# Optimization experiments

Hardware: AMD Instinct MI355X
Metric: run time of the kernel (lower is better)

## Reference

```python
import jax, jax.numpy as jnp
import numpy as np

B, N, D, H = 16, 256, 512, 8
DK = D // H          # 64
DIM_G = 64           # trigonometric geometry embedding dim
WAVE_LEN = 1000.0


def box_relational_embedding(boxes):
    # boxes: [B, N, 4] = (x_min, y_min, x_max, y_max)
    x_min, y_min, x_max, y_max = jnp.split(boxes, 4, axis=-1)  # each [B,N,1]
    cx = ((x_min + x_max) * 0.5)[..., 0]   # [B,N]
    cy = ((y_min + y_max) * 0.5)[..., 0]
    w = (x_max - x_min + 1.0)[..., 0]
    h = (y_max - y_min + 1.0)[..., 0]
    # pairwise deltas, normalized by the *row* box size (as in the torch code)
    dx = jnp.log(jnp.clip(jnp.abs((cx[:, :, None] - cx[:, None, :]) / w[:, :, None]), 1e-3))
    dy = jnp.log(jnp.clip(jnp.abs((cy[:, :, None] - cy[:, None, :]) / h[:, :, None]), 1e-3))
    dw = jnp.log(w[:, :, None] / w[:, None, :])
    dh = jnp.log(h[:, :, None] / h[:, None, :])
    pos = jnp.stack([dx, dy, dw, dh], axis=-1)  # [B,N,N,4]
    # trig embedding: freq per (dim_g/8) channels
    feat_range = jnp.arange(DIM_G // 8, dtype=pos.dtype) / (DIM_G / 8.0)
    dim_mat = 1.0 / jnp.power(WAVE_LEN, feat_range)               # [8]
    mul = (100.0 * pos)[..., None] * dim_mat                      # [B,N,N,4,8]
    mul = mul.reshape(mul.shape[:3] + (-1,))                      # [B,N,N,32]
    return jnp.concatenate([jnp.sin(mul), jnp.cos(mul)], axis=-1)  # [B,N,N,64]


def setup_inputs() -> dict:
    key = jax.random.key(0)
    ks = jax.random.split(key, 16)
    inp = {
        'input_query': jax.random.normal(ks[0], (B, N, D), jnp.float32),
        'input_key': jax.random.normal(ks[1], (B, N, D), jnp.float32),
        'input_value': jax.random.normal(ks[2], (B, N, D), jnp.float32),
    }
    # valid boxes: x_max > x_min, y_max > y_min
    xm = jax.random.uniform(ks[3], (B, N, 1)) * 800.0
    ym = jax.random.uniform(ks[4], (B, N, 1)) * 800.0
    bw = jax.random.uniform(ks[5], (B, N, 1)) * 120.0 + 5.0
    bh = jax.random.uniform(ks[6], (B, N, 1)) * 120.0 + 5.0
    inp['input_box'] = jnp.concatenate([xm, ym, xm + bw, ym + bh], axis=-1)
    s = 1.0 / np.sqrt(D)
    inp['Wq'] = jax.random.normal(ks[7], (D, D), jnp.float32) * s
    inp['bq'] = jnp.zeros((D,), jnp.float32)
    inp['Wk'] = jax.random.normal(ks[8], (D, D), jnp.float32) * s
    inp['bk'] = jnp.zeros((D,), jnp.float32)
    inp['Wv'] = jax.random.normal(ks[9], (D, D), jnp.float32) * s
    inp['bv'] = jnp.zeros((D,), jnp.float32)
    inp['Wo'] = jax.random.normal(ks[10], (D, D), jnp.float32) * s
    inp['bo'] = jnp.zeros((D,), jnp.float32)
    inp['Wg'] = jax.random.normal(ks[11], (H, DIM_G), jnp.float32) * (1.0 / np.sqrt(DIM_G))
    inp['bg'] = jnp.zeros((H,), jnp.float32)
    return inp


def reference(input_query, input_key, input_value, input_box,
              Wq, bq, Wk, bk, Wv, bv, Wo, bo, Wg, bg):
    nb = input_query.shape[0]
    geo = box_relational_embedding(input_box)                     # [B,N,N,64]
    wg = jax.nn.relu(jnp.einsum('bijg,hg->bhij', geo, Wg) + bg[None, :, None, None])
    def proj(x, W, b):
        return (x @ W + b).reshape(nb, -1, H, DK).transpose(0, 2, 1, 3)  # [B,H,N,dk]
    q = proj(input_query, Wq, bq)
    k = proj(input_key, Wk, bk)
    v = proj(input_value, Wv, bv)
    scores = jnp.einsum('bhid,bhjd->bhij', q, k) / np.sqrt(DK)    # [B,H,N,N]
    w_mn = jax.nn.softmax(jnp.log(jnp.clip(wg, 1e-6)) + scores, axis=-1)
    out = jnp.einsum('bhij,bhjd->bhid', w_mn, v)                  # [B,H,N,dk]
    out = out.transpose(0, 2, 1, 3).reshape(nb, -1, H * DK)       # [B,N,D]
    return out @ Wo + bo
```

## Files before the change

kernel.cpp:

```cpp
#include <hip/hip_runtime.h>
#include <hip/hip_bf16.h>

#define B_ 16
#define N_ 256
#define D_ 512
#define H_ 8
#define DK_ 64

typedef unsigned short u16;
typedef __attribute__((ext_vector_type(8))) short bf16x8;
typedef __attribute__((ext_vector_type(4))) float f32x4;

__device__ __forceinline__ float bf2f(u16 u) {
    union { unsigned int i; float f; } v;
    v.i = ((unsigned int)u) << 16;
    return v.f;
}
__device__ __forceinline__ u16 f2bf(float f) {
    union { float f; unsigned int i; } v;
    v.f = f;
    unsigned int x = v.i;
    unsigned int r = (x >> 16) & 1u;
    x += 0x7fffu + r;
    return (u16)(x >> 16);
}

__global__ __launch_bounds__(256) void k_prep(const float* __restrict__ box,
                                              const float* __restrict__ Wg,
                                              const float* __restrict__ bg,
                                              u16* __restrict__ Sg,
                                              const float* __restrict__ W0,
                                              const float* __restrict__ W1,
                                              const float* __restrict__ W2,
                                              const float* __restrict__ W3,
                                              u16* __restrict__ Wt) {
    const int tid = threadIdx.x;
    if (blockIdx.x < 4096) {
        __shared__ float sWg[8][64];
        __shared__ float sbg[8];
        if (tid < 8) sbg[tid] = bg[tid];
        { int e = tid; sWg[e >> 6][e & 63] = Wg[e];
          e = tid + 256; sWg[e >> 6][e & 63] = Wg[e]; }
        const int bi = blockIdx.x, b = bi >> 8;
        float4 bxi = *(const float4*)&box[(size_t)bi * 4];
        float4 bxj = *(const float4*)&box[(size_t)(b * N_ + tid) * 4];
        __syncthreads();
        float cxi = (bxi.x + bxi.z) * 0.5f, cyi = (bxi.y + bxi.w) * 0.5f;
        float wi = bxi.z - bxi.x + 1.0f, hi = bxi.w - bxi.y + 1.0f;
        float cxj = (bxj.x + bxj.z) * 0.5f, cyj = (bxj.y + bxj.w) * 0.5f;
        float wj = bxj.z - bxj.x + 1.0f, hj = bxj.w - bxj.y + 1.0f;
        float pos[4];
        pos[0] = __logf(fmaxf(fabsf((cxi - cxj) / wi), 1e-3f));
        pos[1] = __logf(fmaxf(fabsf((cyi - cyj) / hi), 1e-3f));
        pos[2] = __logf(wi / wj);
        pos[3] = __logf(hi / hj);
        const float dm[8] = {1.0f, 0.42169650342858224f, 0.1778279410038923f,
                             0.07498942093324559f, 0.03162277660168379f,
                             0.013335214321633241f, 0.005623413251903491f,
                             0.0023713737056616554f};
        const float inv2pi = 0.15915494309189535f;
        float acc[8];
#pragma unroll
        for (int h = 0; h < 8; ++h) acc[h] = sbg[h];
#pragma unroll
        for (int t = 0; t < 4; ++t) {
            float base = 100.0f * pos[t];
#pragma unroll
            for (int f = 0; f < 8; ++f) {
                float rev = base * dm[f] * inv2pi;
                rev = rev - floorf(rev);
                float sn = __builtin_amdgcn_sinf(rev);
                float cs = __builtin_amdgcn_cosf(rev);
                int idx = t * 8 + f;
#pragma unroll
                for (int h = 0; h < 8; ++h)
                    acc[h] += sWg[h][idx] * sn + sWg[h][idx + 32] * cs;
            }
        }
        const int i = bi & 255;
#pragma unroll
        for (int h = 0; h < 8; ++h)
            Sg[(((size_t)(b * H_ + h) * N_) + i) * N_ + tid] =
                f2bf(__logf(fmaxf(acc[h], 1e-6f)));
    } else {
        __shared__ float tt[32][33];
        int t = blockIdx.x - 4096;
        int z = t >> 8, yb = (t >> 4) & 15, xb = t & 15;
        const float* W = (z == 0) ? W0 : (z == 1) ? W1 : (z == 2) ? W2 : W3;
        u16* dst = Wt + (size_t)z * 262144;
        const int kb = yb * 32, nb = xb * 32;
#pragma unroll
        for (int r = 0; r < 4; ++r) {
            int p = r * 256 + tid;
            tt[p >> 5][p & 31] = W[(size_t)(kb + (p >> 5)) * 512 + nb + (p & 31)];
        }
        __syncthreads();
#pragma unroll
        for (int r = 0; r < 4; ++r) {
            int p = r * 256 + tid;
            dst[(size_t)(nb + (p >> 5)) * 512 + kb + (p & 31)] = f2bf(tt[p & 31][p >> 5]);
        }
    }
}

__global__ __launch_bounds__(256) void k_gemm_qkv(const float* __restrict__ Xq,
                                                  const float* __restrict__ Xk,
                                                  const float* __restrict__ Xv,
                                                  const u16* __restrict__ Wtb,
                                                  const float* __restrict__ bq,
                                                  const float* __restrict__ bk,
                                                  const float* __restrict__ bv,
                                                  u16* __restrict__ qkv) {
    const int z = blockIdx.z;
    const float* A = (z == 0) ? Xq : (z == 1) ? Xk : Xv;
    const u16* Wt = Wtb + (size_t)z * 262144;
    const float* bias = (z == 0) ? bq : (z == 1) ? bk : bv;
    u16* dst = qkv + (size_t)z * 2097152;

    __shared__ u16 As[2][64][72];
    __shared__ u16 Bs[2][64][72];
    const int tid = threadIdx.x;
    const int n0 = blockIdx.x * 64, m0 = blockIdx.y * 64;
    const int wid = tid >> 6, lane = tid & 63;
    const int wm = (wid & 1) * 32, wn = (wid >> 1) * 32;
    const int lr = lane & 15, lk8 = (lane >> 4) * 8, quad4 = (lane >> 4) * 4;

    f32x4 acc[2][2];
#pragma unroll
    for (int mi = 0; mi < 2; ++mi)
#pragma unroll
        for (int ni = 0; ni < 2; ++ni) acc[mi][ni] = (f32x4){0.f, 0.f, 0.f, 0.f};

    float4 raf[4];
    ushort4 rb[4];
#pragma unroll
    for (int r = 0; r < 4; ++r) {
        int p = r * 256 + tid, row = p >> 4, c4 = (p & 15) * 4;
        raf[r] = *(const float4*)&A[(size_t)(m0 + row) * 512 + c4];
        rb[r] = *(const ushort4*)&Wt[(size_t)(n0 + row) * 512 + c4];
    }
#pragma unroll
    for (int r = 0; r < 4; ++r) {
        int p = r * 256 + tid, row = p >> 4, c4 = (p & 15) * 4;
        ushort4 ab;
        ab.x = f2bf(raf[r].x); ab.y = f2bf(raf[r].y);
        ab.z = f2bf(raf[r].z); ab.w = f2bf(raf[r].w);
        *(ushort4*)&As[0][row][c4] = ab;
        *(ushort4*)&Bs[0][row][c4] = rb[r];
    }
    __syncthreads();
    for (int it = 0; it < 8; ++it) {
        const int cur = it & 1;
        if (it < 7) {
            int k0n = (it + 1) * 64;
#pragma unroll
            for (int r = 0; r < 4; ++r) {
                int p = r * 256 + tid, row = p >> 4, c4 = (p & 15) * 4;
                raf[r] = *(const float4*)&A[(size_t)(m0 + row) * 512 + k0n + c4];
                rb[r] = *(const ushort4*)&Wt[(size_t)(n0 + row) * 512 + k0n + c4];
            }
        }
#pragma unroll
        for (int ks = 0; ks < 64; ks += 32) {
            bf16x8 af[2], bfx[2];
#pragma unroll
            for (int mi = 0; mi < 2; ++mi)
                af[mi] = *(const bf16x8*)&As[cur][wm + mi * 16 + lr][ks + lk8];
#pragma unroll
            for (int ni = 0; ni < 2; ++ni)
                bfx[ni] = *(const bf16x8*)&Bs[cur][wn + ni * 16 + lr][ks + lk8];
#pragma unroll
            for (int mi = 0; mi < 2; ++mi)
#pragma unroll
                for (int ni = 0; ni < 2; ++ni)
                    acc[mi][ni] = __builtin_amdgcn_mfma_f32_16x16x32_bf16(
                        af[mi], bfx[ni], acc[mi][ni], 0, 0, 0);
        }
        if (it < 7) {
#pragma unroll
            for (int r = 0; r < 4; ++r) {
                int p = r * 256 + tid, row = p >> 4, c4 = (p & 15) * 4;
                ushort4 ab;
                ab.x = f2bf(raf[r].x); ab.y = f2bf(raf[r].y);
                ab.z = f2bf(raf[r].z); ab.w = f2bf(raf[r].w);
                *(ushort4*)&As[1 - cur][row][c4] = ab;
                *(ushort4*)&Bs[1 - cur][row][c4] = rb[r];
            }
            __syncthreads();
        }
    }
    u16* bounce = &As[0][0][0];
    const float scale = (z == 0) ? 0.125f : 1.0f;
    const int h = n0 >> 6, b = m0 >> 8, rrb = m0 & 255;
    if (z == 2) {
#pragma unroll
        for (int mi = 0; mi < 2; ++mi)
#pragma unroll
            for (int ni = 0; ni < 2; ++ni) {
                int cn = wn + ni * 16 + lr;
                float bb = bias[n0 + cn];
#pragma unroll
                for (int reg = 0; reg < 4; ++reg) {
                    int rm = wm + mi * 16 + quad4 + reg;
                    bounce[cn * 72 + rm] = f2bf(acc[mi][ni][reg] + bb);
                }
            }
        __syncthreads();
#pragma unroll
        for (int r = 0; r < 4; ++r) {
            int p = r * 256 + tid, dn = p >> 4, c4 = (p & 15) * 4;
            *(ushort4*)&dst[(((size_t)(b * H_ + h) * DK_) + dn) * N_ + rrb + c4] =
                *(const ushort4*)&bounce[dn * 72 + c4];
        }
    } else {
#pragma unroll
        for (int mi = 0; mi < 2; ++mi)
#pragma unroll
            for (int ni = 0; ni < 2; ++ni) {
                int cn = wn + ni * 16 + lr;
                float bb = bias[n0 + cn];
#pragma unroll
                for (int reg = 0; reg < 4; ++reg) {
                    int rm = wm + mi * 16 + quad4 + reg;
                    bounce[rm * 72 + cn] = f2bf((acc[mi][ni][reg] + bb) * scale);
                }
            }
        __syncthreads();
#pragma unroll
        for (int r = 0; r < 4; ++r) {
            int p = r * 256 + tid, rm = p >> 4, c4 = (p & 15) * 4;
            *(ushort4*)&dst[(((size_t)(b * H_ + h) * N_) + rrb + rm) * DK_ + c4] =
                *(const ushort4*)&bounce[rm * 72 + c4];
        }
    }
}

__global__ __launch_bounds__(256) void k_gemm_out(const u16* __restrict__ Ab,
                                                  const u16* __restrict__ Wt,
                                                  const float* __restrict__ bias,
                                                  float* __restrict__ outp) {
    __shared__ u16 As[2][64][72];
    __shared__ u16 Bs[2][64][72];
    const int tid = threadIdx.x;
    const int n0 = blockIdx.x * 64, m0 = blockIdx.y * 64;
    const int wid = tid >> 6, lane = tid & 63;
    const int wm = (wid & 1) * 32, wn = (wid >> 1) * 32;
    const int lr = lane & 15, lk8 = (lane >> 4) * 8;
    f32x4 acc[2][2];
#pragma unroll
    for (int mi = 0; mi < 2; ++mi)
#pragma unroll
        for (int ni = 0; ni < 2; ++ni) acc[mi][ni] = (f32x4){0.f, 0.f, 0.f, 0.f};
    ushort4 ra[4], rb[4];
#pragma unroll
    for (int r = 0; r < 4; ++r) {
        int p = r * 256 + tid, row = p >> 4, c4 = (p & 15) * 4;
        ra[r] = *(const ushort4*)&Ab[(size_t)(m0 + row) * 512 + c4];
        rb[r] = *(const ushort4*)&Wt[(size_t)(n0 + row) * 512 + c4];
    }
#pragma unroll
    for (int r = 0; r < 4; ++r) {
        int p = r * 256 + tid, row = p >> 4, c4 = (p & 15) * 4;
        *(ushort4*)&As[0][row][c4] = ra[r];
        *(ushort4*)&Bs[0][row][c4] = rb[r];
    }
    __syncthreads();
    for (int it = 0; it < 8; ++it) {
        const int cur = it & 1;
        if (it < 7) {
            int k0n = (it + 1) * 64;
#pragma unroll
            for (int r = 0; r < 4; ++r) {
                int p = r * 256 + tid, row = p >> 4, c4 = (p & 15) * 4;
                ra[r] = *(const ushort4*)&Ab[(size_t)(m0 + row) * 512 + k0n + c4];
                rb[r] = *(const ushort4*)&Wt[(size_t)(n0 + row) * 512 + k0n + c4];
            }
        }
#pragma unroll
        for (int ks = 0; ks < 64; ks += 32) {
            bf16x8 af[2], bfx[2];
#pragma unroll
            for (int mi = 0; mi < 2; ++mi)
                af[mi] = *(const bf16x8*)&As[cur][wm + mi * 16 + lr][ks + lk8];
#pragma unroll
            for (int ni = 0; ni < 2; ++ni)
                bfx[ni] = *(const bf16x8*)&Bs[cur][wn + ni * 16 + lr][ks + lk8];
#pragma unroll
            for (int mi = 0; mi < 2; ++mi)
#pragma unroll
                for (int ni = 0; ni < 2; ++ni)
                    acc[mi][ni] = __builtin_amdgcn_mfma_f32_16x16x32_bf16(
                        af[mi], bfx[ni], acc[mi][ni], 0, 0, 0);
        }
        if (it < 7) {
#pragma unroll
            for (int r = 0; r < 4; ++r) {
                int p = r * 256 + tid, row = p >> 4, c4 = (p & 15) * 4;
                *(ushort4*)&As[1 - cur][row][c4] = ra[r];
                *(ushort4*)&Bs[1 - cur][row][c4] = rb[r];
            }
            __syncthreads();
        }
    }
#pragma unroll
    for (int mi = 0; mi < 2; ++mi)
#pragma unroll
        for (int ni = 0; ni < 2; ++ni) {
            int col = n0 + wn + ni * 16 + lr;
            float bb = bias[col];
#pragma unroll
            for (int reg = 0; reg < 4; ++reg) {
                int m = m0 + wm + mi * 16 + (lane >> 4) * 4 + reg;
                outp[(size_t)m * 512 + col] = acc[mi][ni][reg] + bb;
            }
        }
}

__global__ __launch_bounds__(256) void k_attn(const u16* __restrict__ qh,
                                              const u16* __restrict__ kh,
                                              const u16* __restrict__ vhT,
                                              const u16* __restrict__ Sg,
                                              u16* __restrict__ attnb) {
    __shared__ __align__(16) unsigned char smem[40960];
    u16* sQ = (u16*)smem;
    u16* sP = (u16*)(smem + 4608);
    u16* sK = (u16*)(smem + 21504);
    u16* sVt = (u16*)(smem + 21504);
    float* sRedM = (float*)(smem + 39936);
    float* sRedS = (float*)(smem + 40448);

    const int tid = threadIdx.x;
    const int i0 = blockIdx.x * 32;
    const int bh = blockIdx.y;
    const int b = bh >> 3, h = bh & 7;
    const int wid = tid >> 6, lane = tid & 63;
    const int lr = lane & 15, lk8 = (lane >> 4) * 8, quad4 = (lane >> 4) * 4;

#pragma unroll
    for (int r = 0; r < 2; ++r) {
        int p = r * 256 + tid, i = p >> 4, d0 = (p & 15) * 4;
        *(ushort4*)&sQ[i * 72 + d0] =
            *(const ushort4*)&qh[((size_t)bh * N_ + i0 + i) * DK_ + d0];
    }
#pragma unroll
    for (int r = 0; r < 8; ++r) {
        int p = r * 256 + tid, row = p >> 6, jc = (p & 63) * 4;
        *(ushort4*)&sP[row * 264 + jc] =
            *(const ushort4*)&Sg[(((size_t)bh * N_) + i0 + row) * N_ + jc];
    }
#pragma unroll
    for (int r = 0; r < 8; ++r) {
        int p = r * 256 + tid, j = p >> 4, d0 = (p & 15) * 4;
        *(ushort4*)&sK[j * 72 + d0] =
            *(const ushort4*)&kh[((size_t)bh * N_ + j) * DK_ + d0];
    }
    __syncthreads();

    ushort4 kpre[8];
#pragma unroll
    for (int r = 0; r < 8; ++r) {
        int p = r * 256 + tid, j = p >> 4, d0 = (p & 15) * 4;
        kpre[r] = *(const ushort4*)&kh[((size_t)bh * N_ + 128 + j) * DK_ + d0];
    }
    f32x4 acc[2][2][2];
#pragma unroll
    for (int c = 0; c < 2; ++c)
#pragma unroll
        for (int mi = 0; mi < 2; ++mi)
#pragma unroll
            for (int ni = 0; ni < 2; ++ni) acc[c][mi][ni] = (f32x4){0.f, 0.f, 0.f, 0.f};
#pragma unroll
    for (int ks = 0; ks < 64; ks += 32) {
        bf16x8 af[2], bfx[2];
#pragma unroll
        for (int mi = 0; mi < 2; ++mi)
            af[mi] = *(const bf16x8*)&sQ[(mi * 16 + lr) * 72 + ks + lk8];
#pragma unroll
        for (int ni = 0; ni < 2; ++ni)
            bfx[ni] = *(const bf16x8*)&sK[(wid * 32 + ni * 16 + lr) * 72 + ks + lk8];
#pragma unroll
        for (int mi = 0; mi < 2; ++mi)
#pragma unroll
            for (int ni = 0; ni < 2; ++ni)
                acc[0][mi][ni] = __builtin_amdgcn_mfma_f32_16x16x32_bf16(
                    af[mi], bfx[ni], acc[0][mi][ni], 0, 0, 0);
    }
    __syncthreads();
#pragma unroll
    for (int r = 0; r < 8; ++r) {
        int p = r * 256 + tid, j = p >> 4, d0 = (p & 15) * 4;
        *(ushort4*)&sK[j * 72 + d0] = kpre[r];
    }
    __syncthreads();
#pragma unroll
    for (int ks = 0; ks < 64; ks += 32) {
        bf16x8 af[2], bfx[2];
#pragma unroll
        for (int mi = 0; mi < 2; ++mi)
            af[mi] = *(const bf16x8*)&sQ[(mi * 16 + lr) * 72 + ks + lk8];
#pragma unroll
        for (int ni = 0; ni < 2; ++ni)
            bfx[ni] = *(const bf16x8*)&sK[(wid * 32 + ni * 16 + lr) * 72 + ks + lk8];
#pragma unroll
        for (int mi = 0; mi < 2; ++mi)
#pragma unroll
            for (int ni = 0; ni < 2; ++ni)
                acc[1][mi][ni] = __builtin_amdgcn_mfma_f32_16x16x32_bf16(
                    af[mi], bfx[ni], acc[1][mi][ni], 0, 0, 0);
    }
    __syncthreads();

#pragma unroll
    for (int r = 0; r < 8; ++r) {
        int p = r * 256 + tid, d = p >> 5, jc = (p & 31) * 4;
        *(ushort4*)&sVt[d * 136 + jc] =
            *(const ushort4*)&vhT[(((size_t)bh * DK_) + d) * N_ + jc];
    }
#pragma unroll
    for (int c = 0; c < 2; ++c)
#pragma unroll
        for (int mi = 0; mi < 2; ++mi)
#pragma unroll
            for (int ni = 0; ni < 2; ++ni) {
                int col = c * 128 + wid * 32 + ni * 16 + lr;
#pragma unroll
                for (int reg = 0; reg < 4; ++reg) {
                    int row = mi * 16 + quad4 + reg;
                    acc[c][mi][ni][reg] += bf2f(sP[row * 264 + col]);
                }
            }
    float mrow[2][4];
#pragma unroll
    for (int mi = 0; mi < 2; ++mi)
#pragma unroll
        for (int reg = 0; reg < 4; ++reg) {
            float m = acc[0][mi][0][reg];
            m = fmaxf(m, acc[0][mi][1][reg]);
            m = fmaxf(m, acc[1][mi][0][reg]);
            m = fmaxf(m, acc[1][mi][1][reg]);
#pragma unroll
            for (int off = 1; off <= 8; off <<= 1) m = fmaxf(m, __shfl_xor(m, off, 64));
            mrow[mi][reg] = m;
        }
    if (lr == 0) {
#pragma unroll
        for (int mi = 0; mi < 2; ++mi)
#pragma unroll
            for (int reg = 0; reg < 4; ++reg)
                sRedM[(mi * 16 + quad4 + reg) * 4 + wid] = mrow[mi][reg];
    }
    __syncthreads();
    float gm[2][4], sl[2][4];
#pragma unroll
    for (int mi = 0; mi < 2; ++mi)
#pragma unroll
        for (int reg = 0; reg < 4; ++reg) {
            float4 mm = *(const float4*)&sRedM[(mi * 16 + quad4 + reg) * 4];
            gm[mi][reg] = fmaxf(fmaxf(mm.x, mm.y), fmaxf(mm.z, mm.w));
            sl[mi][reg] = 0.f;
        }
#pragma unroll
    for (int c = 0; c < 2; ++c)
#pragma unroll
        for (int mi = 0; mi < 2; ++mi)
#pragma unroll
            for (int ni = 0; ni < 2; ++ni)
#pragma unroll
                for (int reg = 0; reg < 4; ++reg) {
                    float e = __expf(acc[c][mi][ni][reg] - gm[mi][reg]);
                    acc[c][mi][ni][reg] = e;
                    sl[mi][reg] += e;
                }
#pragma unroll
    for (int mi = 0; mi < 2; ++mi)
#pragma unroll
        for (int reg = 0; reg < 4; ++reg) {
            float s = sl[mi][reg];
#pragma unroll
            for (int off = 1; off <= 8; off <<= 1) s += __shfl_xor(s, off, 64);
            sl[mi][reg] = s;
        }
    if (lr == 0) {
#pragma unroll
        for (int mi = 0; mi < 2; ++mi)
#pragma unroll
            for (int reg = 0; reg < 4; ++reg)
                sRedS[(mi * 16 + quad4 + reg) * 4 + wid] = sl[mi][reg];
    }
    __syncthreads();
#pragma unroll
    for (int mi = 0; mi < 2; ++mi)
#pragma unroll
        for (int reg = 0; reg < 4; ++reg) {
            float4 ss = *(const float4*)&sRedS[(mi * 16 + quad4 + reg) * 4];
            gm[mi][reg] = 1.0f / (ss.x + ss.y + ss.z + ss.w);
        }
#pragma unroll
    for (int c = 0; c < 2; ++c)
#pragma unroll
        for (int mi = 0; mi < 2; ++mi)
#pragma unroll
            for (int ni = 0; ni < 2; ++ni) {
                int col = c * 128 + wid * 32 + ni * 16 + lr;
#pragma unroll
                for (int reg = 0; reg < 4; ++reg) {
                    int row = mi * 16 + quad4 + reg;
                    sP[row * 264 + col] = f2bf(acc[c][mi][ni][reg] * gm[mi][reg]);
                }
            }
    __syncthreads();

    f32x4 o[2];
    o[0] = (f32x4){0.f, 0.f, 0.f, 0.f};
    o[1] = (f32x4){0.f, 0.f, 0.f, 0.f};
#pragma unroll
    for (int k0 = 0; k0 < 128; k0 += 32) {
        bf16x8 bfx = *(const bf16x8*)&sVt[(wid * 16 + lr) * 136 + k0 + lk8];
#pragma unroll
        for (int mi = 0; mi < 2; ++mi) {
            bf16x8 af = *(const bf16x8*)&sP[(mi * 16 + lr) * 264 + k0 + lk8];
            o[mi] = __builtin_amdgcn_mfma_f32_16x16x32_bf16(af, bfx, o[mi], 0, 0, 0);
        }
    }
    __syncthreads();
#pragma unroll
    for (int r = 0; r < 8; ++r) {
        int p = r * 256 + tid, d = p >> 5, jc = (p & 31) * 4;
        *(ushort4*)&sVt[d * 136 + jc] =
            *(const ushort4*)&vhT[(((size_t)bh * DK_) + d) * N_ + 128 + jc];
    }
    __syncthreads();
#pragma unroll
    for (int k0 = 0; k0 < 128; k0 += 32) {
        bf16x8 bfx = *(const bf16x8*)&sVt[(wid * 16 + lr) * 136 + k0 + lk8];
#pragma unroll
        for (int mi = 0; mi < 2; ++mi) {
            bf16x8 af = *(const bf16x8*)&sP[(mi * 16 + lr) * 264 + 128 + k0 + lk8];
            o[mi] = __builtin_amdgcn_mfma_f32_16x16x32_bf16(af, bfx, o[mi], 0, 0, 0);
        }
    }
#pragma unroll
    for (int mi = 0; mi < 2; ++mi)
#pragma unroll
        for (int reg = 0; reg < 4; ++reg) {
            int row = mi * 16 + quad4 + reg;
            attnb[((size_t)(b * N_ + i0 + row)) * D_ + h * 64 + wid * 16 + lr] =
                f2bf(o[mi][reg]);
        }
}

extern "C" void kernel_launch(void* const* d_in, const int* in_sizes, int n_in,
                              void* d_out, int out_size, void* d_ws, size_t ws_size,
                              hipStream_t stream) {
    const float* Xq = (const float*)d_in[0];
    const float* Xk = (const float*)d_in[1];
    const float* Xv = (const float*)d_in[2];
    const float* box = (const float*)d_in[3];
    const float* Wq = (const float*)d_in[4];
    const float* bq = (const float*)d_in[5];
    const float* Wk = (const float*)d_in[6];
    const float* bk = (const float*)d_in[7];
    const float* Wv = (const float*)d_in[8];
    const float* bv = (const float*)d_in[9];
    const float* Wo = (const float*)d_in[10];
    const float* bo = (const float*)d_in[11];
    const float* Wg = (const float*)d_in[12];
    const float* bg = (const float*)d_in[13];
    float* out = (float*)d_out;

    u16* ws16 = (u16*)d_ws;
    u16* qkv = ws16;
    u16* qh = qkv;
    u16* kh = qkv + 2097152;
    u16* vhT = qkv + 4194304;
    u16* Sg = ws16 + 6291456;
    u16* attnb = ws16 + 14680064;
    u16* Wt = ws16 + 16777216;

    dim3 blk(256);
    k_prep<<<dim3(5120), blk, 0, stream>>>(box, Wg, bg, Sg, Wq, Wk, Wv, Wo, Wt);
    k_gemm_qkv<<<dim3(8, 64, 3), blk, 0, stream>>>(Xq, Xk, Xv, Wt, bq, bk, bv, qkv);
    k_attn<<<dim3(8, 128), blk, 0, stream>>>(qh, kh, vhT, Sg, attnb);
    k_gemm_out<<<dim3(8, 64), blk, 0, stream>>>(attnb, Wt + 3 * 262144, bo, out);
}
```

Baseline: 179.5 us.

## Enlarge GEMM M-tile to 128 and switch to single-buffered shared memory

The QKV and output-projection GEMMs now compute 128x64 tiles per block instead of 64x64. Each warp holds a 64x32 sub-tile, so every B-fragment load is reused across twice as many MFMAs. Shared memory drops from double to single buffering, with global-to-register prefetch kept and a second barrier added per k-step. The grids are halved accordingly, which reduces the number of blocks in flight and adds a sync stall in exchange for better reuse.

```diff
diff --git a/kernel.cpp b/kernel.cpp
--- a/kernel.cpp
+++ b/kernel.cpp
@@ -117,84 +117,83 @@
     const float* bias = (z == 0) ? bq : (z == 1) ? bk : bv;
     u16* dst = qkv + (size_t)z * 2097152;
 
-    __shared__ u16 As[2][64][72];
-    __shared__ u16 Bs[2][64][72];
+    __shared__ u16 As[128][72];
+    __shared__ u16 Bs[64][72];
     const int tid = threadIdx.x;
-    const int n0 = blockIdx.x * 64, m0 = blockIdx.y * 64;
+    const int n0 = blockIdx.x * 64, m0 = blockIdx.y * 128;
     const int wid = tid >> 6, lane = tid & 63;
-    const int wm = (wid & 1) * 32, wn = (wid >> 1) * 32;
+    const int wm = (wid & 1) * 64, wn = (wid >> 1) * 32;
     const int lr = lane & 15, lk8 = (lane >> 4) * 8, quad4 = (lane >> 4) * 4;
 
-    f32x4 acc[2][2];
-#pragma unroll
-    for (int mi = 0; mi < 2; ++mi)
+    f32x4 acc[4][2];
+#pragma unroll
+    for (int mi = 0; mi < 4; ++mi)
 #pragma unroll
         for (int ni = 0; ni < 2; ++ni) acc[mi][ni] = (f32x4){0.f, 0.f, 0.f, 0.f};
 
-    float4 raf[4];
+    float4 raf[8];
     ushort4 rb[4];
 #pragma unroll
-    for (int r = 0; r < 4; ++r) {
+    for (int r = 0; r < 8; ++r) {
         int p = r * 256 + tid, row = p >> 4, c4 = (p & 15) * 4;
         raf[r] = *(const float4*)&A[(size_t)(m0 + row) * 512 + c4];
-        rb[r] = *(const ushort4*)&Wt[(size_t)(n0 + row) * 512 + c4];
     }
 #pragma unroll
     for (int r = 0; r < 4; ++r) {
-        int p = r * 256 + tid, row = p >> 4, c4 = (p & 15) * 4;
-        ushort4 ab;
-        ab.x = f2bf(raf[r].x); ab.y = f2bf(raf[r].y);
-        ab.z = f2bf(raf[r].z); ab.w = f2bf(raf[r].w);
-        *(ushort4*)&As[0][row][c4] = ab;
-        *(ushort4*)&Bs[0][row][c4] = rb[r];
-    }
-    __syncthreads();
+        int p = r * 256 + tid, n = p >> 4, c4 = (p & 15) * 4;
+        rb[r] = *(const ushort4*)&Wt[(size_t)(n0 + n) * 512 + c4];
+    }
     for (int it = 0; it < 8; ++it) {
-        const int cur = it & 1;
+#pragma unroll
+        for (int r = 0; r < 8; ++r) {
+            int p = r * 256 + tid, row = p >> 4, c4 = (p & 15) * 4;
+            ushort4 ab;
+            ab.x = f2bf(raf[r].x); ab.y = f2bf(raf[r].y);
+            ab.z = f2bf(raf[r].z); ab.w = f2bf(raf[r].w);
+            *(ushort4*)&As[row][c4] = ab;
+        }
+#pragma unroll
+        for (int r = 0; r < 4; ++r) {
+            int p = r * 256 + tid, n = p >> 4, c4 = (p & 15) * 4;
+            *(ushort4*)&Bs[n][c4] = rb[r];
+        }
+        __syncthreads();
         if (it < 7) {
             int k0n = (it + 1) * 64;
 #pragma unroll
-            for (int r = 0; r < 4; ++r) {
+            for (int r = 0; r < 8; ++r) {
                 int p = r * 256 + tid, row = p >> 4, c4 = (p & 15) * 4;
                 raf[r] = *(const float4*)&A[(size_t)(m0 + row) * 512 + k0n + c4];
-                rb[r] = *(const ushort4*)&Wt[(size_t)(n0 + row) * 512 + k0n + c4];
+            }
+#pragma unroll
+            for (int r = 0; r < 4; ++r) {
+                int p = r * 256 + tid, n = p >> 4, c4 = (p & 15) * 4;
+                rb[r] = *(const ushort4*)&Wt[(size_t)(n0 + n) * 512 + k0n + c4];
             }
         }
 #pragma unroll
         for (int ks = 0; ks < 64; ks += 32) {
-            bf16x8 af[2], bfx[2];
-#pragma unroll
-            for (int mi = 0; mi < 2; ++mi)
-                af[mi] = *(const bf16x8*)&As[cur][wm + mi * 16 + lr][ks + lk8];
+            bf16x8 af[4], bfx[2];
+#pragma unroll
+            for (int mi = 0; mi < 4; ++mi)
+                af[mi] = *(const bf16x8*)&As[wm + mi * 16 + lr][ks + lk8];
 #pragma unroll
             for (int ni = 0; ni < 2; ++ni)
-                bfx[ni] = *(const bf16x8*)&Bs[cur][wn + ni * 16 + lr][ks + lk8];
-#pragma unroll
-            for (int mi = 0; mi < 2; ++mi)
+                bfx[ni] = *(const bf16x8*)&Bs[wn + ni * 16 + lr][ks + lk8];
+#pragma unroll
+            for (int mi = 0; mi < 4; ++mi)
 #pragma unroll
                 for (int ni = 0; ni < 2; ++ni)
                     acc[mi][ni] = __builtin_amdgcn_mfma_f32_16x16x32_bf16(
                         af[mi], bfx[ni], acc[mi][ni], 0, 0, 0);
         }
-        if (it < 7) {
-#pragma unroll
-            for (int r = 0; r < 4; ++r) {
-                int p = r * 256 + tid, row = p >> 4, c4 = (p & 15) * 4;
-                ushort4 ab;
-                ab.x = f2bf(raf[r].x); ab.y = f2bf(raf[r].y);
-                ab.z = f2bf(raf[r].z); ab.w = f2bf(raf[r].w);
-                *(ushort4*)&As[1 - cur][row][c4] = ab;
-                *(ushort4*)&Bs[1 - cur][row][c4] = rb[r];
-            }
-            __syncthreads();
-        }
-    }
-    u16* bounce = &As[0][0][0];
-    const float scale = (z == 0) ? 0.125f : 1.0f;
+        __syncthreads();
+    }
     const int h = n0 >> 6, b = m0 >> 8, rrb = m0 & 255;
     if (z == 2) {
-#pragma unroll
-        for (int mi = 0; mi < 2; ++mi)
+        u16* bounce = &As[0][0];
+#pragma unroll
+        for (int mi = 0; mi < 4; ++mi)
 #pragma unroll
             for (int ni = 0; ni < 2; ++ni) {
                 int cn = wn + ni * 16 + lr;
@@ -202,19 +201,21 @@
 #pragma unroll
                 for (int reg = 0; reg < 4; ++reg) {
                     int rm = wm + mi * 16 + quad4 + reg;
-                    bounce[cn * 72 + rm] = f2bf(acc[mi][ni][reg] + bb);
+                    bounce[cn * 136 + rm] = f2bf(acc[mi][ni][reg] + bb);
                 }
             }
         __syncthreads();
 #pragma unroll
-        for (int r = 0; r < 4; ++r) {
-            int p = r * 256 + tid, dn = p >> 4, c4 = (p & 15) * 4;
+        for (int r = 0; r < 8; ++r) {
+            int p = r * 256 + tid, dn = p >> 5, c4 = (p & 31) * 4;
             *(ushort4*)&dst[(((size_t)(b * H_ + h) * DK_) + dn) * N_ + rrb + c4] =
-                *(const ushort4*)&bounce[dn * 72 + c4];
+                *(const ushort4*)&bounce[dn * 136 + c4];
         }
     } else {
-#pragma unroll
-        for (int mi = 0; mi < 2; ++mi)
+        u16* bounce = &As[0][0];
+        const float scale = (z == 0) ? 0.125f : 1.0f;
+#pragma unroll
+        for (int mi = 0; mi < 4; ++mi)
 #pragma unroll
             for (int ni = 0; ni < 2; ++ni) {
                 int cn = wn + ni * 16 + lr;
@@ -227,7 +228,7 @@
             }
         __syncthreads();
 #pragma unroll
-        for (int r = 0; r < 4; ++r) {
+        for (int r = 0; r < 8; ++r) {
             int p = r * 256 + tid, rm = p >> 4, c4 = (p & 15) * 4;
             *(ushort4*)&dst[(((size_t)(b * H_ + h) * N_) + rrb + rm) * DK_ + c4] =
                 *(const ushort4*)&bounce[rm * 72 + c4];
@@ -239,71 +240,74 @@
                                                   const u16* __restrict__ Wt,
                                                   const float* __restrict__ bias,
                                                   float* __restrict__ outp) {
-    __shared__ u16 As[2][64][72];
-    __shared__ u16 Bs[2][64][72];
+    __shared__ u16 As[128][72];
+    __shared__ u16 Bs[64][72];
     const int tid = threadIdx.x;
-    const int n0 = blockIdx.x * 64, m0 = blockIdx.y * 64;
+    const int n0 = blockIdx.x * 64, m0 = blockIdx.y * 128;
     const int wid = tid >> 6, lane = tid & 63;
-    const int wm = (wid & 1) * 32, wn = (wid >> 1) * 32;
+    const int wm = (wid & 1) * 64, wn = (wid >> 1) * 32;
     const int lr = lane & 15, lk8 = (lane >> 4) * 8;
-    f32x4 acc[2][2];
-#pragma unroll
-    for (int mi = 0; mi < 2; ++mi)
+    f32x4 acc[4][2];
+#pragma unroll
+    for (int mi = 0; mi < 4; ++mi)
 #pragma unroll
         for (int ni = 0; ni < 2; ++ni) acc[mi][ni] = (f32x4){0.f, 0.f, 0.f, 0.f};
-    ushort4 ra[4], rb[4];
-#pragma unroll
-    for (int r = 0; r < 4; ++r) {
+    ushort4 ra[8], rb[4];
+#pragma unroll
+    for (int r = 0; r < 8; ++r) {
         int p = r * 256 + tid, row = p >> 4, c4 = (p & 15) * 4;
         ra[r] = *(const ushort4*)&Ab[(size_t)(m0 + row) * 512 + c4];
-        rb[r] = *(const ushort4*)&Wt[(size_t)(n0 + row) * 512 + c4];
     }
 #pragma unroll
     for (int r = 0; r < 4; ++r) {
-        int p = r * 256 + tid, row = p >> 4, c4 = (p & 15) * 4;
-        *(ushort4*)&As[0][row][c4] = ra[r];
-        *(ushort4*)&Bs[0][row][c4] = rb[r];
-    }
-    __syncthreads();
+        int p = r * 256 + tid, n = p >> 4, c4 = (p & 15) * 4;
+        rb[r] = *(const ushort4*)&Wt[(size_t)(n0 + n) * 512 + c4];
+    }
     for (int it = 0; it < 8; ++it) {
-        const int cur = it & 1;
+#pragma unroll
+        for (int r = 0; r < 8; ++r) {
+            int p = r * 256 + tid, row = p >> 4, c4 = (p & 15) * 4;
+            *(ushort4*)&As[row][c4] = ra[r];
+        }
+#pragma unroll
+        for (int r = 0; r < 4; ++r) {
+            int p = r * 256 + tid, n = p >> 4, c4 = (p & 15) * 4;
+            *(ushort4*)&Bs[n][c4] = rb[r];
+        }
+        __syncthreads();
         if (it < 7) {
             int k0n = (it + 1) * 64;
 #pragma unroll
-            for (int r = 0; r < 4; ++r) {
+            for (int r = 0; r < 8; ++r) {
                 int p = r * 256 + tid, row = p >> 4, c4 = (p & 15) * 4;
                 ra[r] = *(const ushort4*)&Ab[(size_t)(m0 + row) * 512 + k0n + c4];
-                rb[r] = *(const ushort4*)&Wt[(size_t)(n0 + row) * 512 + k0n + c4];
+            }
+#pragma unroll
+            for (int r = 0; r < 4; ++r) {
+                int p = r * 256 + tid, n = p >> 4, c4 = (p & 15) * 4;
+                rb[r] = *(const ushort4*)&Wt[(size_t)(n0 + n) * 512 + k0n + c4];
             }
         }
 #pragma unroll
         for (int ks = 0; ks < 64; ks += 32) {
-            bf16x8 af[2], bfx[2];
-#pragma unroll
-            for (int mi = 0; mi < 2; ++mi)
-                af[mi] = *(const bf16x8*)&As[cur][wm + mi * 16 + lr][ks + lk8];
+            bf16x8 af[4], bfx[2];
+#pragma unroll
+            for (int mi = 0; mi < 4; ++mi)
+                af[mi] = *(const bf16x8*)&As[wm + mi * 16 + lr][ks + lk8];
 #pragma unroll
             for (int ni = 0; ni < 2; ++ni)
-                bfx[ni] = *(const bf16x8*)&Bs[cur][wn + ni * 16 + lr][ks + lk8];
-#pragma unroll
-            for (int mi = 0; mi < 2; ++mi)
+                bfx[ni] = *(const bf16x8*)&Bs[wn + ni * 16 + lr][ks + lk8];
+#pragma unroll
+            for (int mi = 0; mi < 4; ++mi)
 #pragma unroll
                 for (int ni = 0; ni < 2; ++ni)
                     acc[mi][ni] = __builtin_amdgcn_mfma_f32_16x16x32_bf16(
                         af[mi], bfx[ni], acc[mi][ni], 0, 0, 0);
         }
-        if (it < 7) {
-#pragma unroll
-            for (int r = 0; r < 4; ++r) {
-                int p = r * 256 + tid, row = p >> 4, c4 = (p & 15) * 4;
-                *(ushort4*)&As[1 - cur][row][c4] = ra[r];
-                *(ushort4*)&Bs[1 - cur][row][c4] = rb[r];
-            }
-            __syncthreads();
-        }
-    }
-#pragma unroll
-    for (int mi = 0; mi < 2; ++mi)
+        __syncthreads();
+    }
+#pragma unroll
+    for (int mi = 0; mi < 4; ++mi)
 #pragma unroll
         for (int ni = 0; ni < 2; ++ni) {
             int col = n0 + wn + ni * 16 + lr;
@@ -579,7 +583,7 @@
 
     dim3 blk(256);
     k_prep<<<dim3(5120), blk, 0, stream>>>(box, Wg, bg, Sg, Wq, Wk, Wv, Wo, Wt);
-    k_gemm_qkv<<<dim3(8, 64, 3), blk, 0, stream>>>(Xq, Xk, Xv, Wt, bq, bk, bv, qkv);
+    k_gemm_qkv<<<dim3(8, 32, 3), blk, 0, stream>>>(Xq, Xk, Xv, Wt, bq, bk, bv, qkv);
     k_attn<<<dim3(8, 128), blk, 0, stream>>>(qh, kh, vhT, Sg, attnb);
-    k_gemm_out<<<dim3(8, 64), blk, 0, stream>>>(attnb, Wt + 3 * 262144, bo, out);
-}
+    k_gemm_out<<<dim3(8, 32), blk, 0, stream>>>(attnb, Wt + 3 * 262144, bo, out);
+}
```

Result: no change. 181.6 us (+1.1%).

## Fuse QKV GEMM with geometry prep and drop the weight pre-transpose

Applied to the files above, without the earlier changes.

Merges the QKV projection GEMM and the box-geometry bias computation into one launch, with block index choosing the role. The separate weight transpose/bf16 pass is removed: both GEMMs now read fp32 weights directly, convert them to bf16 and store them transposed into shared memory with a padded stride. This cuts one kernel launch and a full round trip of the weights through global memory. In exchange, the B-tile shared stores become scalar, possibly bank-conflicting writes, and each block repeats the weight conversion.

```diff
diff --git a/kernel.cpp b/kernel.cpp
--- a/kernel.cpp
+++ b/kernel.cpp
@@ -25,23 +25,159 @@
     return (u16)(x >> 16);
 }
 
-__global__ __launch_bounds__(256) void k_prep(const float* __restrict__ box,
-                                              const float* __restrict__ Wg,
-                                              const float* __restrict__ bg,
-                                              u16* __restrict__ Sg,
-                                              const float* __restrict__ W0,
-                                              const float* __restrict__ W1,
-                                              const float* __restrict__ W2,
-                                              const float* __restrict__ W3,
-                                              u16* __restrict__ Wt) {
+__global__ __launch_bounds__(256) void k_fused1(const float* __restrict__ Xq,
+                                                const float* __restrict__ Xk,
+                                                const float* __restrict__ Xv,
+                                                const float* __restrict__ Wq,
+                                                const float* __restrict__ Wk,
+                                                const float* __restrict__ Wv,
+                                                const float* __restrict__ bq,
+                                                const float* __restrict__ bk,
+                                                const float* __restrict__ bv,
+                                                const float* __restrict__ box,
+                                                const float* __restrict__ Wg,
+                                                const float* __restrict__ bg,
+                                                u16* __restrict__ qkv,
+                                                u16* __restrict__ Sg) {
+    __shared__ __align__(16) unsigned char smem[35328];
     const int tid = threadIdx.x;
-    if (blockIdx.x < 4096) {
-        __shared__ float sWg[8][64];
-        __shared__ float sbg[8];
+    const int bid = blockIdx.x;
+    if (bid < 1536) {
+        u16* As = (u16*)smem;
+        u16* Bs = (u16*)(smem + 18432);
+        const int z = bid >> 9, t = bid & 511;
+        const int m0 = (t >> 3) * 64, n0 = (t & 7) * 64;
+        const float* A = (z == 0) ? Xq : (z == 1) ? Xk : Xv;
+        const float* W = (z == 0) ? Wq : (z == 1) ? Wk : Wv;
+        const float* bias = (z == 0) ? bq : (z == 1) ? bk : bv;
+        u16* dst = qkv + (size_t)z * 2097152;
+        const int wid = tid >> 6, lane = tid & 63;
+        const int wm = (wid & 1) * 32, wn = (wid >> 1) * 32;
+        const int lr = lane & 15, lk8 = (lane >> 4) * 8, quad4 = (lane >> 4) * 4;
+
+        f32x4 acc[2][2];
+#pragma unroll
+        for (int mi = 0; mi < 2; ++mi)
+#pragma unroll
+            for (int ni = 0; ni < 2; ++ni) acc[mi][ni] = (f32x4){0.f, 0.f, 0.f, 0.f};
+
+        float4 raf[4], rwf[4];
+#pragma unroll
+        for (int r = 0; r < 4; ++r) {
+            int p = r * 256 + tid, row = p >> 4, c4 = (p & 15) * 4;
+            raf[r] = *(const float4*)&A[(size_t)(m0 + row) * 512 + c4];
+            rwf[r] = *(const float4*)&W[(size_t)row * 512 + n0 + c4];
+        }
+#pragma unroll
+        for (int r = 0; r < 4; ++r) {
+            int p = r * 256 + tid, row = p >> 4, c4 = (p & 15) * 4;
+            ushort4 ab;
+            ab.x = f2bf(raf[r].x); ab.y = f2bf(raf[r].y);
+            ab.z = f2bf(raf[r].z); ab.w = f2bf(raf[r].w);
+            *(ushort4*)&As[row * 72 + c4] = ab;
+            Bs[(c4 + 0) * 66 + row] = f2bf(rwf[r].x);
+            Bs[(c4 + 1) * 66 + row] = f2bf(rwf[r].y);
+            Bs[(c4 + 2) * 66 + row] = f2bf(rwf[r].z);
+            Bs[(c4 + 3) * 66 + row] = f2bf(rwf[r].w);
+        }
+        __syncthreads();
+        for (int it = 0; it < 8; ++it) {
+            const int cur = it & 1;
+            if (it < 7) {
+                int k0n = (it + 1) * 64;
+#pragma unroll
+                for (int r = 0; r < 4; ++r) {
+                    int p = r * 256 + tid, row = p >> 4, c4 = (p & 15) * 4;
+                    raf[r] = *(const float4*)&A[(size_t)(m0 + row) * 512 + k0n + c4];
+                    rwf[r] = *(const float4*)&W[(size_t)(k0n + row) * 512 + n0 + c4];
+                }
+            }
+#pragma unroll
+            for (int ks = 0; ks < 64; ks += 32) {
+                bf16x8 af[2], bfx[2];
+#pragma unroll
+                for (int mi = 0; mi < 2; ++mi)
+                    af[mi] = *(const bf16x8*)&As[(cur * 64 + wm + mi * 16 + lr) * 72 + ks + lk8];
+#pragma unroll
+                for (int ni = 0; ni < 2; ++ni)
+                    bfx[ni] = *(const bf16x8*)&Bs[(cur * 64 + wn + ni * 16 + lr) * 66 + ks + lk8];
+#pragma unroll
+                for (int mi = 0; mi < 2; ++mi)
+#pragma unroll
+                    for (int ni = 0; ni < 2; ++ni)
+                        acc[mi][ni] = __builtin_amdgcn_mfma_f32_16x16x32_bf16(
+                            af[mi], bfx[ni], acc[mi][ni], 0, 0, 0);
+            }
+            if (it < 7) {
+                const int nxt = 1 - cur;
+#pragma unroll
+                for (int r = 0; r < 4; ++r) {
+                    int p = r * 256 + tid, row = p >> 4, c4 = (p & 15) * 4;
+                    ushort4 ab;
+                    ab.x = f2bf(raf[r].x); ab.y = f2bf(raf[r].y);
+                    ab.z = f2bf(raf[r].z); ab.w = f2bf(raf[r].w);
+                    *(ushort4*)&As[(nxt * 64 + row) * 72 + c4] = ab;
+                    Bs[(nxt * 64 + c4 + 0) * 66 + row] = f2bf(rwf[r].x);
+                    Bs[(nxt * 64 + c4 + 1) * 66 + row] = f2bf(rwf[r].y);
+                    Bs[(nxt * 64 + c4 + 2) * 66 + row] = f2bf(rwf[r].z);
+                    Bs[(nxt * 64 + c4 + 3) * 66 + row] = f2bf(rwf[r].w);
+                }
+                __syncthreads();
+            }
+        }
+        __syncthreads();
+        const int h = n0 >> 6, b = m0 >> 8, rrb = m0 & 255;
+        if (z == 2) {
+            u16* bounce = (u16*)smem;
+#pragma unroll
+            for (int mi = 0; mi < 2; ++mi)
+#pragma unroll
+                for (int ni = 0; ni < 2; ++ni) {
+                    int cn = wn + ni * 16 + lr;
+                    float bb = bias[n0 + cn];
+#pragma unroll
+                    for (int reg = 0; reg < 4; ++reg) {
+                        int rm = wm + mi * 16 + quad4 + reg;
+                        bounce[cn * 136 + rm] = f2bf(acc[mi][ni][reg] + bb);
+                    }
+                }
+            __syncthreads();
+#pragma unroll
+            for (int r = 0; r < 4; ++r) {
+                int p = r * 256 + tid, dn = p >> 4, c4 = (p & 15) * 4;
+                *(ushort4*)&dst[(((size_t)(b * H_ + h) * DK_) + dn) * N_ + rrb + c4] =
+                    *(const ushort4*)&bounce[dn * 136 + c4];
+            }
+        } else {
+            u16* bounce = (u16*)smem;
+            const float scale = (z == 0) ? 0.125f : 1.0f;
+#pragma unroll
+            for (int mi = 0; mi < 2; ++mi)
+#pragma unroll
+                for (int ni = 0; ni < 2; ++ni) {
+                    int cn = wn + ni * 16 + lr;
+                    float bb = bias[n0 + cn];
+#pragma unroll
+                    for (int reg = 0; reg < 4; ++reg) {
+                        int rm = wm + mi * 16 + quad4 + reg;
+                        bounce[rm * 72 + cn] = f2bf((acc[mi][ni][reg] + bb) * scale);
+                    }
+                }
+            __syncthreads();
+#pragma unroll
+            for (int r = 0; r < 4; ++r) {
+                int p = r * 256 + tid, rm = p >> 4, c4 = (p & 15) * 4;
+                *(ushort4*)&dst[(((size_t)(b * H_ + h) * N_) + rrb + rm) * DK_ + c4] =
+                    *(const ushort4*)&bounce[rm * 72 + c4];
+            }
+        }
+    } else {
+        float* sWg = (float*)smem;
+        float* sbg = (float*)(smem + 2048);
         if (tid < 8) sbg[tid] = bg[tid];
-        { int e = tid; sWg[e >> 6][e & 63] = Wg[e];
-          e = tid + 256; sWg[e >> 6][e & 63] = Wg[e]; }
-        const int bi = blockIdx.x, b = bi >> 8;
+        { int e = tid; sWg[(e >> 6) * 64 + (e & 63)] = Wg[e];
+          e = tid + 256; sWg[(e >> 6) * 64 + (e & 63)] = Wg[e]; }
+        const int bi = bid - 1536, b = bi >> 8;
         float4 bxi = *(const float4*)&box[(size_t)bi * 4];
         float4 bxj = *(const float4*)&box[(size_t)(b * N_ + tid) * 4];
         __syncthreads();
@@ -74,7 +210,7 @@
                 int idx = t * 8 + f;
 #pragma unroll
                 for (int h = 0; h < 8; ++h)
-                    acc[h] += sWg[h][idx] * sn + sWg[h][idx + 32] * cs;
+                    acc[h] += sWg[h * 64 + idx] * sn + sWg[h * 64 + idx + 32] * cs;
             }
         }
         const int i = bi & 255;
@@ -82,165 +218,16 @@
         for (int h = 0; h < 8; ++h)
             Sg[(((size_t)(b * H_ + h) * N_) + i) * N_ + tid] =
                 f2bf(__logf(fmaxf(acc[h], 1e-6f)));
-    } else {
-        __shared__ float tt[32][33];
-        int t = blockIdx.x - 4096;
-        int z = t >> 8, yb = (t >> 4) & 15, xb = t & 15;
-        const float* W = (z == 0) ? W0 : (z == 1) ? W1 : (z == 2) ? W2 : W3;
-        u16* dst = Wt + (size_t)z * 262144;
-        const int kb = yb * 32, nb = xb * 32;
-#pragma unroll
-        for (int r = 0; r < 4; ++r) {
-            int p = r * 256 + tid;
-            tt[p >> 5][p & 31] = W[(size_t)(kb + (p >> 5)) * 512 + nb + (p & 31)];
-        }
-        __syncthreads();
-#pragma unroll
-        for (int r = 0; r < 4; ++r) {
-            int p = r * 256 + tid;
-            dst[(size_t)(nb + (p >> 5)) * 512 + kb + (p & 31)] = f2bf(tt[p & 31][p >> 5]);
-        }
     }
 }
 
-__global__ __launch_bounds__(256) void k_gemm_qkv(const float* __restrict__ Xq,
-                                                  const float* __restrict__ Xk,
-                                                  const float* __restrict__ Xv,
-                                                  const u16* __restrict__ Wtb,
-                                                  const float* __restrict__ bq,
-                                                  const float* __restrict__ bk,
-                                                  const float* __restrict__ bv,
-                                                  u16* __restrict__ qkv) {
-    const int z = blockIdx.z;
-    const float* A = (z == 0) ? Xq : (z == 1) ? Xk : Xv;
-    const u16* Wt = Wtb + (size_t)z * 262144;
-    const float* bias = (z == 0) ? bq : (z == 1) ? bk : bv;
-    u16* dst = qkv + (size_t)z * 2097152;
-
-    __shared__ u16 As[2][64][72];
-    __shared__ u16 Bs[2][64][72];
-    const int tid = threadIdx.x;
-    const int n0 = blockIdx.x * 64, m0 = blockIdx.y * 64;
-    const int wid = tid >> 6, lane = tid & 63;
-    const int wm = (wid & 1) * 32, wn = (wid >> 1) * 32;
-    const int lr = lane & 15, lk8 = (lane >> 4) * 8, quad4 = (lane >> 4) * 4;
-
-    f32x4 acc[2][2];
-#pragma unroll
-    for (int mi = 0; mi < 2; ++mi)
-#pragma unroll
-        for (int ni = 0; ni < 2; ++ni) acc[mi][ni] = (f32x4){0.f, 0.f, 0.f, 0.f};
-
-    float4 raf[4];
-    ushort4 rb[4];
-#pragma unroll
-    for (int r = 0; r < 4; ++r) {
-        int p = r * 256 + tid, row = p >> 4, c4 = (p & 15) * 4;
-        raf[r] = *(const float4*)&A[(size_t)(m0 + row) * 512 + c4];
-        rb[r] = *(const ushort4*)&Wt[(size_t)(n0 + row) * 512 + c4];
-    }
-#pragma unroll
-    for (int r = 0; r < 4; ++r) {
-        int p = r * 256 + tid, row = p >> 4, c4 = (p & 15) * 4;
-        ushort4 ab;
-        ab.x = f2bf(raf[r].x); ab.y = f2bf(raf[r].y);
-        ab.z = f2bf(raf[r].z); ab.w = f2bf(raf[r].w);
-        *(ushort4*)&As[0][row][c4] = ab;
-        *(ushort4*)&Bs[0][row][c4] = rb[r];
-    }
-    __syncthreads();
-    for (int it = 0; it < 8; ++it) {
-        const int cur = it & 1;
-        if (it < 7) {
-            int k0n = (it + 1) * 64;
-#pragma unroll
-            for (int r = 0; r < 4; ++r) {
-                int p = r * 256 + tid, row = p >> 4, c4 = (p & 15) * 4;
-                raf[r] = *(const float4*)&A[(size_t)(m0 + row) * 512 + k0n + c4];
-                rb[r] = *(const ushort4*)&Wt[(size_t)(n0 + row) * 512 + k0n + c4];
-            }
-        }
-#pragma unroll
-        for (int ks = 0; ks < 64; ks += 32) {
-            bf16x8 af[2], bfx[2];
-#pragma unroll
-            for (int mi = 0; mi < 2; ++mi)
-                af[mi] = *(const bf16x8*)&As[cur][wm + mi * 16 + lr][ks + lk8];
-#pragma unroll
-            for (int ni = 0; ni < 2; ++ni)
-                bfx[ni] = *(const bf16x8*)&Bs[cur][wn + ni * 16 + lr][ks + lk8];
-#pragma unroll
-            for (int mi = 0; mi < 2; ++mi)
-#pragma unroll
-                for (int ni = 0; ni < 2; ++ni)
-                    acc[mi][ni] = __builtin_amdgcn_mfma_f32_16x16x32_bf16(
-                        af[mi], bfx[ni], acc[mi][ni], 0, 0, 0);
-        }
-        if (it < 7) {
-#pragma unroll
-            for (int r = 0; r < 4; ++r) {
-                int p = r * 256 + tid, row = p >> 4, c4 = (p & 15) * 4;
-                ushort4 ab;
-                ab.x = f2bf(raf[r].x); ab.y = f2bf(raf[r].y);
-                ab.z = f2bf(raf[r].z); ab.w = f2bf(raf[r].w);
-                *(ushort4*)&As[1 - cur][row][c4] = ab;
-                *(ushort4*)&Bs[1 - cur][row][c4] = rb[r];
-            }
-            __syncthreads();
-        }
-    }
-    u16* bounce = &As[0][0][0];
-    const float scale = (z == 0) ? 0.125f : 1.0f;
-    const int h = n0 >> 6, b = m0 >> 8, rrb = m0 & 255;
-    if (z == 2) {
-#pragma unroll
-        for (int mi = 0; mi < 2; ++mi)
-#pragma unroll
-            for (int ni = 0; ni < 2; ++ni) {
-                int cn = wn + ni * 16 + lr;
-                float bb = bias[n0 + cn];
-#pragma unroll
-                for (int reg = 0; reg < 4; ++reg) {
-                    int rm = wm + mi * 16 + quad4 + reg;
-                    bounce[cn * 72 + rm] = f2bf(acc[mi][ni][reg] + bb);
-                }
-            }
-        __syncthreads();
-#pragma unroll
-        for (int r = 0; r < 4; ++r) {
-            int p = r * 256 + tid, dn = p >> 4, c4 = (p & 15) * 4;
-            *(ushort4*)&dst[(((size_t)(b * H_ + h) * DK_) + dn) * N_ + rrb + c4] =
-                *(const ushort4*)&bounce[dn * 72 + c4];
-        }
-    } else {
-#pragma unroll
-        for (int mi = 0; mi < 2; ++mi)
-#pragma unroll
-            for (int ni = 0; ni < 2; ++ni) {
-                int cn = wn + ni * 16 + lr;
-                float bb = bias[n0 + cn];
-#pragma unroll
-                for (int reg = 0; reg < 4; ++reg) {
-                    int rm = wm + mi * 16 + quad4 + reg;
-                    bounce[rm * 72 + cn] = f2bf((acc[mi][ni][reg] + bb) * scale);
-                }
-            }
-        __syncthreads();
-#pragma unroll
-        for (int r = 0; r < 4; ++r) {
-            int p = r * 256 + tid, rm = p >> 4, c4 = (p & 15) * 4;
-            *(ushort4*)&dst[(((size_t)(b * H_ + h) * N_) + rrb + rm) * DK_ + c4] =
-                *(const ushort4*)&bounce[rm * 72 + c4];
-        }
-    }
-}
-
 __global__ __launch_bounds__(256) void k_gemm_out(const u16* __restrict__ Ab,
-                                                  const u16* __restrict__ Wt,
+                                                  const float* __restrict__ W,
                                                   const float* __restrict__ bias,
                                                   float* __restrict__ outp) {
-    __shared__ u16 As[2][64][72];
-    __shared__ u16 Bs[2][64][72];
+    __shared__ __align__(16) unsigned char smem[35328];
+    u16* As = (u16*)smem;
+    u16* Bs = (u16*)(smem + 18432);
     const int tid = threadIdx.x;
     const int n0 = blockIdx.x * 64, m0 = blockIdx.y * 64;
     const int wid = tid >> 6, lane = tid & 63;
@@ -251,18 +238,22 @@
     for (int mi = 0; mi < 2; ++mi)
 #pragma unroll
         for (int ni = 0; ni < 2; ++ni) acc[mi][ni] = (f32x4){0.f, 0.f, 0.f, 0.f};
-    ushort4 ra[4], rb[4];
+    ushort4 ra[4];
+    float4 rwf[4];
 #pragma unroll
     for (int r = 0; r < 4; ++r) {
         int p = r * 256 + tid, row = p >> 4, c4 = (p & 15) * 4;
         ra[r] = *(const ushort4*)&Ab[(size_t)(m0 + row) * 512 + c4];
-        rb[r] = *(const ushort4*)&Wt[(size_t)(n0 + row) * 512 + c4];
+        rwf[r] = *(const float4*)&W[(size_t)row * 512 + n0 + c4];
     }
 #pragma unroll
     for (int r = 0; r < 4; ++r) {
         int p = r * 256 + tid, row = p >> 4, c4 = (p & 15) * 4;
-        *(ushort4*)&As[0][row][c4] = ra[r];
-        *(ushort4*)&Bs[0][row][c4] = rb[r];
+        *(ushort4*)&As[row * 72 + c4] = ra[r];
+        Bs[(c4 + 0) * 66 + row] = f2bf(rwf[r].x);
+        Bs[(c4 + 1) * 66 + row] = f2bf(rwf[r].y);
+        Bs[(c4 + 2) * 66 + row] = f2bf(rwf[r].z);
+        Bs[(c4 + 3) * 66 + row] = f2bf(rwf[r].w);
     }
     __syncthreads();
     for (int it = 0; it < 8; ++it) {
@@ -273,7 +264,7 @@
             for (int r = 0; r < 4; ++r) {
                 int p = r * 256 + tid, row = p >> 4, c4 = (p & 15) * 4;
                 ra[r] = *(const ushort4*)&Ab[(size_t)(m0 + row) * 512 + k0n + c4];
-                rb[r] = *(const ushort4*)&Wt[(size_t)(n0 + row) * 512 + k0n + c4];
+                rwf[r] = *(const float4*)&W[(size_t)(k0n + row) * 512 + n0 + c4];
             }
         }
 #pragma unroll
@@ -281,10 +272,10 @@
             bf16x8 af[2], bfx[2];
 #pragma unroll
             for (int mi = 0; mi < 2; ++mi)
-                af[mi] = *(const bf16x8*)&As[cur][wm + mi * 16 + lr][ks + lk8];
+                af[mi] = *(const bf16x8*)&As[(cur * 64 + wm + mi * 16 + lr) * 72 + ks + lk8];
 #pragma unroll
             for (int ni = 0; ni < 2; ++ni)
-                bfx[ni] = *(const bf16x8*)&Bs[cur][wn + ni * 16 + lr][ks + lk8];
+                bfx[ni] = *(const bf16x8*)&Bs[(cur * 64 + wn + ni * 16 + lr) * 66 + ks + lk8];
 #pragma unroll
             for (int mi = 0; mi < 2; ++mi)
 #pragma unroll
@@ -293,11 +284,15 @@
                         af[mi], bfx[ni], acc[mi][ni], 0, 0, 0);
         }
         if (it < 7) {
+            const int nxt = 1 - cur;
 #pragma unroll
             for (int r = 0; r < 4; ++r) {
                 int p = r * 256 + tid, row = p >> 4, c4 = (p & 15) * 4;
-                *(ushort4*)&As[1 - cur][row][c4] = ra[r];
-                *(ushort4*)&Bs[1 - cur][row][c4] = rb[r];
+                *(ushort4*)&As[(nxt * 64 + row) * 72 + c4] = ra[r];
+                Bs[(nxt * 64 + c4 + 0) * 66 + row] = f2bf(rwf[r].x);
+                Bs[(nxt * 64 + c4 + 1) * 66 + row] = f2bf(rwf[r].y);
+                Bs[(nxt * 64 + c4 + 2) * 66 + row] = f2bf(rwf[r].z);
+                Bs[(nxt * 64 + c4 + 3) * 66 + row] = f2bf(rwf[r].w);
             }
             __syncthreads();
         }
@@ -575,11 +570,10 @@
     u16* vhT = qkv + 4194304;
     u16* Sg = ws16 + 6291456;
     u16* attnb = ws16 + 14680064;
-    u16* Wt = ws16 + 16777216;
 
     dim3 blk(256);
-    k_prep<<<dim3(5120), blk, 0, stream>>>(box, Wg, bg, Sg, Wq, Wk, Wv, Wo, Wt);
-    k_gemm_qkv<<<dim3(8, 64, 3), blk, 0, stream>>>(Xq, Xk, Xv, Wt, bq, bk, bv, qkv);
+    k_fused1<<<dim3(5632), blk, 0, stream>>>(Xq, Xk, Xv, Wq, Wk, Wv, bq, bk, bv,
+                                             box, Wg, bg, qkv, Sg);
     k_attn<<<dim3(8, 128), blk, 0, stream>>>(qh, kh, vhT, Sg, attnb);
-    k_gemm_out<<<dim3(8, 64), blk, 0, stream>>>(attnb, Wt + 3 * 262144, bo, out);
+    k_gemm_out<<<dim3(8, 64), blk, 0, stream>>>(attnb, Wo, bo, out);
 }
```

New measurement: 196.4 us. 1.09x slower.
